# Optimization experiments

Measured on AMD Instinct MI355X. Metric: run time of the kernel, lower is better.

The kernel has to match this reference:

```python
import jax, jax.numpy as jnp
import numpy as np
import math

IN_DIM = 128
OUT_DIM = 128
EDGE_DIM = 16
LN_EPS = 1e-5


def setup_inputs() -> dict:
    key = jax.random.key(0)
    ks = jax.random.split(key, 6)
    bs, N = 8, 512
    x = jax.random.normal(ks[0], (bs, N, IN_DIM), dtype=jnp.float32)
    edge_feats = jax.random.normal(ks[1], (bs, N, N, EDGE_DIM), dtype=jnp.float32)
    # fc weight (out_dim, in_dim), xavier-uniform scale
    lim_w = math.sqrt(6.0 / (IN_DIM + OUT_DIM))
    W = jax.random.uniform(ks[2], (OUT_DIM, IN_DIM), minval=-lim_w, maxval=lim_w, dtype=jnp.float32)
    # attn_fc weight (1, 2*out_dim+edge_dim) split into a_src | a_dst | a_e
    fan_in = 2 * OUT_DIM + EDGE_DIM
    lim_a = math.sqrt(6.0 / (fan_in + 1))
    a = jax.random.uniform(ks[3], (fan_in,), minval=-lim_a, maxval=lim_a, dtype=jnp.float32)
    a_src, a_dst, a_e = a[:OUT_DIM], a[OUT_DIM:2 * OUT_DIM], a[2 * OUT_DIM:]
    gamma = jnp.ones((OUT_DIM,), dtype=jnp.float32)
    beta = jnp.zeros((OUT_DIM,), dtype=jnp.float32)
    return {"x": x, "edge_feats": edge_feats, "W": W, "a_src": a_src,
            "a_dst": a_dst, "a_e": a_e, "gamma": gamma, "beta": beta}


def reference(x, edge_feats, W, a_src, a_dst, a_e, gamma, beta):
    # h: (bs, N, out_dim)
    h = jnp.einsum('bni,oi->bno', x, W)
    scale = 1.0 / math.sqrt(OUT_DIM)
    # Decomposed rank-1 attention score: attn_fc([h_i, h_j, e_ij]) =
    # h_i.a_src + h_j.a_dst + e_ij.a_e  -- identical math, no (bs,N,N,2D+E) tensor.
    s_i = jnp.einsum('bnd,d->bn', h, a_src)           # row term (index i)
    s_j = jnp.einsum('bnd,d->bn', h, a_dst)           # col term (index j)
    s_e = jnp.einsum('bije,e->bij', edge_feats, a_e)  # edge term
    e_ij = (s_i[:, :, None] + s_j[:, None, :] + s_e) * scale  # (bs, N, N)
    # max-subtract then softmax over j (jax.nn.softmax is already max-stable,
    # and softmax(e - max) == softmax(e))
    alpha = jax.nn.softmax(e_ij, axis=-1)
    # weighted sum over neighbors j (dropout skipped: eval mode)
    h_prime = jnp.einsum('bij,bjd->bid', alpha, h)
    # LayerNorm over last dim
    mu = jnp.mean(h_prime, axis=-1, keepdims=True)
    var = jnp.var(h_prime, axis=-1, keepdims=True)
    out = (h_prime - mu) * jax.lax.rsqrt(var + LN_EPS) * gamma + beta
    return out
```

## Files before the change

### kernel.cpp

```cpp
#include <hip/hip_runtime.h>
#include <math.h>

#define NB 8
#define NN 512
#define D 128
#define TIF 4
#define K1R 8
#define LN_EPS 1e-5f
#define SCALE 0.08838834764831845f

typedef float f32x4 __attribute__((ext_vector_type(4)));

__device__ __forceinline__ float dotv(f32x4 a, f32x4 b) {
    f32x4 m = a * b;
    return m.x + m.y + m.z + m.w;
}
__device__ __forceinline__ float dot4(float4 a, float4 b) {
    return a.x * b.x + a.y * b.y + a.z * b.z + a.w * b.w;
}

__global__ __launch_bounds__(256) void k1_proj(
    const float* __restrict__ x, const float* __restrict__ W,
    const float* __restrict__ a_src, const float* __restrict__ a_dst,
    float* __restrict__ h_ws, float* __restrict__ si_ws, float* __restrict__ sj_ws)
{
    __shared__ __align__(16) float4 Wl[128][32];
    __shared__ __align__(16) float4 xl[K1R][32];
    __shared__ float redk[K1R][2][2];

    const int t = threadIdx.x;
    const int row0 = blockIdx.x * K1R;

    const float4* Wg = (const float4*)W;
#pragma unroll
    for (int k = 0; k < 16; ++k) {
        const int f = t + 256 * k;
        const int o = f >> 5, q = f & 31;
        Wl[o][q ^ (o & 7)] = Wg[f];
    }
    xl[t >> 5][t & 31] = ((const float4*)(x + (size_t)row0 * D))[t];
    __syncthreads();

    const int o = t & 127;
    const int rb = (t >> 7) * (K1R / 2);
    float acc[K1R / 2] = {0.f, 0.f, 0.f, 0.f};
#pragma unroll
    for (int q = 0; q < 32; ++q) {
        const float4 wv = Wl[o][q ^ (o & 7)];
#pragma unroll
        for (int r = 0; r < K1R / 2; ++r) acc[r] += dot4(wv, xl[rb + r][q]);
    }
    const float as = a_src[o], ad = a_dst[o];
#pragma unroll
    for (int r = 0; r < K1R / 2; ++r) {
        h_ws[(size_t)(row0 + rb + r) * D + o] = acc[r];
        float vs = acc[r] * as, vd = acc[r] * ad;
#pragma unroll
        for (int m = 32; m >= 1; m >>= 1) {
            vs += __shfl_xor(vs, m);
            vd += __shfl_xor(vd, m);
        }
        if ((t & 63) == 0) {
            redk[rb + r][0][(t >> 6) & 1] = vs;
            redk[rb + r][1][(t >> 6) & 1] = vd;
        }
    }
    __syncthreads();
    if (t < K1R) si_ws[row0 + t] = redk[t][0][0] + redk[t][0][1];
    else if (t < 2 * K1R) {
        const int r = t - K1R;
        sj_ws[row0 + r] = redk[r][1][0] + redk[r][1][1];
    }
}

__global__ __launch_bounds__(256, 4) void kfused(
    const float* __restrict__ ef, const float* __restrict__ a_e,
    const float* __restrict__ gamma, const float* __restrict__ beta,
    const float* __restrict__ h_ws, const float* __restrict__ si_ws,
    const float* __restrict__ sj_ws, float* __restrict__ out)
{
    __shared__ float sj_l[NN];
    __shared__ __align__(16) float sa[TIF][NN];
    __shared__ __align__(16) float part[4][TIF][D];
    __shared__ float redm[TIF][2];
    __shared__ float reds[TIF][2];

    const int t = threadIdx.x;
    const int w = t >> 6;
    const int lane = t & 63;
    const int bid = blockIdx.x;
    const int b = bid >> 7;
    const int i0 = (bid & 127) * TIF;

    sj_l[t] = sj_ws[b * NN + t];
    sj_l[t + 256] = sj_ws[b * NN + t + 256];

    const int c = t & 3;
    const f32x4 A = ((const f32x4*)a_e)[c];
    const f32x4* ef4 = (const f32x4*)ef + ((size_t)b * NN + i0) * NN * 4;
    float* saf = &sa[0][0];
#pragma unroll 8
    for (int k = 0; k < 32; ++k) {
        const int f = 256 * k + t;
        const f32x4 v = ef4[f];
        float p = dotv(v, A);
        p += __shfl_xor(p, 1);
        p += __shfl_xor(p, 2);
        if (c == 0) saf[f >> 2] = p;
    }
    __syncthreads();

    const int q = t & 127;
    const int rp = t >> 7;
    const int r0 = 2 * rp, r1 = 2 * rp + 1;
    const int wh = (t >> 6) & 1;
    const float si0 = si_ws[b * NN + i0 + r0];
    const float si1 = si_ws[b * NN + i0 + r1];
    const f32x4 sjv = *(const f32x4*)&sj_l[4 * q];
    const f32x4 e0 = (si0 + sjv + *(const f32x4*)&sa[r0][4 * q]) * SCALE;
    const f32x4 e1 = (si1 + sjv + *(const f32x4*)&sa[r1][4 * q]) * SCALE;
    float m0 = fmaxf(fmaxf(e0.x, e0.y), fmaxf(e0.z, e0.w));
    float m1 = fmaxf(fmaxf(e1.x, e1.y), fmaxf(e1.z, e1.w));
#pragma unroll
    for (int mm = 32; mm >= 1; mm >>= 1) {
        m0 = fmaxf(m0, __shfl_xor(m0, mm));
        m1 = fmaxf(m1, __shfl_xor(m1, mm));
    }
    if (lane == 0) { redm[r0][wh] = m0; redm[r1][wh] = m1; }
    __syncthreads();

    {
        const float mx0 = fmaxf(redm[r0][0], redm[r0][1]);
        const float mx1 = fmaxf(redm[r1][0], redm[r1][1]);
        f32x4 a0, a1;
        a0.x = __expf(e0.x - mx0); a0.y = __expf(e0.y - mx0);
        a0.z = __expf(e0.z - mx0); a0.w = __expf(e0.w - mx0);
        a1.x = __expf(e1.x - mx1); a1.y = __expf(e1.y - mx1);
        a1.z = __expf(e1.z - mx1); a1.w = __expf(e1.w - mx1);
        *(f32x4*)&sa[r0][4 * q] = a0;
        *(f32x4*)&sa[r1][4 * q] = a1;
        float s0 = a0.x + a0.y + a0.z + a0.w;
        float s1 = a1.x + a1.y + a1.z + a1.w;
#pragma unroll
        for (int mm = 32; mm >= 1; mm >>= 1) {
            s0 += __shfl_xor(s0, mm);
            s1 += __shfl_xor(s1, mm);
        }
        if (lane == 0) { reds[r0][wh] = s0; reds[r1][wh] = s1; }
    }
    __syncthreads();

    const int dl = (t & 31) << 2;
    const int g = t >> 5;
    float acc[TIF][4];
#pragma unroll
    for (int r = 0; r < TIF; ++r)
#pragma unroll
        for (int cc = 0; cc < 4; ++cc) acc[r][cc] = 0.f;

    const float* hb = h_ws + (size_t)b * NN * D;
#pragma unroll 2
    for (int jt = 0; jt < 16; ++jt) {
        const int j0 = (g << 6) + (jt << 2);
        float4 hv0 = *(const float4*)(hb + (size_t)(j0 + 0) * D + dl);
        float4 hv1 = *(const float4*)(hb + (size_t)(j0 + 1) * D + dl);
        float4 hv2 = *(const float4*)(hb + (size_t)(j0 + 2) * D + dl);
        float4 hv3 = *(const float4*)(hb + (size_t)(j0 + 3) * D + dl);
#pragma unroll
        for (int r = 0; r < TIF; ++r) {
            const f32x4 av = *(const f32x4*)&sa[r][j0];
            acc[r][0] += av.x * hv0.x + av.y * hv1.x + av.z * hv2.x + av.w * hv3.x;
            acc[r][1] += av.x * hv0.y + av.y * hv1.y + av.z * hv2.y + av.w * hv3.y;
            acc[r][2] += av.x * hv0.z + av.y * hv1.z + av.z * hv2.z + av.w * hv3.z;
            acc[r][3] += av.x * hv0.w + av.y * hv1.w + av.z * hv2.w + av.w * hv3.w;
        }
    }
#pragma unroll
    for (int r = 0; r < TIF; ++r)
#pragma unroll
        for (int cc = 0; cc < 4; ++cc) acc[r][cc] += __shfl_xor(acc[r][cc], 32);
    if (lane < 32) {
#pragma unroll
        for (int r = 0; r < TIF; ++r)
            *(float4*)&part[w][r][dl] = make_float4(acc[r][0], acc[r][1], acc[r][2], acc[r][3]);
    }
    __syncthreads();

    {
        const int r = w;
        const float inv = 1.0f / (reds[r][0] + reds[r][1]);
        const int d0 = lane, d1 = lane + 64;
        float v0 = 0.f, v1 = 0.f;
#pragma unroll
        for (int pw = 0; pw < 4; ++pw) {
            v0 += part[pw][r][d0];
            v1 += part[pw][r][d1];
        }
        v0 *= inv; v1 *= inv;
        float s = v0 + v1, qq = v0 * v0 + v1 * v1;
#pragma unroll
        for (int mm = 32; mm >= 1; mm >>= 1) {
            s += __shfl_xor(s, mm);
            qq += __shfl_xor(qq, mm);
        }
        const float mu = s * (1.f / 128.f);
        const float var = qq * (1.f / 128.f) - mu * mu;
        const float rs = rsqrtf(var + LN_EPS);
        const size_t ob = ((size_t)(b * NN + i0 + r)) * D;
        out[ob + d0] = (v0 - mu) * rs * gamma[d0] + beta[d0];
        out[ob + d1] = (v1 - mu) * rs * gamma[d1] + beta[d1];
    }
}

extern "C" void kernel_launch(void* const* d_in, const int* in_sizes, int n_in,
                              void* d_out, int out_size, void* d_ws, size_t ws_size,
                              hipStream_t stream) {
    const float* x     = (const float*)d_in[0];
    const float* ef    = (const float*)d_in[1];
    const float* W     = (const float*)d_in[2];
    const float* a_src = (const float*)d_in[3];
    const float* a_dst = (const float*)d_in[4];
    const float* a_e   = (const float*)d_in[5];
    const float* gamma = (const float*)d_in[6];
    const float* beta  = (const float*)d_in[7];
    float* out = (float*)d_out;

    float* h_ws  = (float*)d_ws;
    float* si_ws = h_ws + (size_t)NB * NN * D;
    float* sj_ws = si_ws + NB * NN;

    k1_proj<<<NB * NN / K1R, 256, 0, stream>>>(x, W, a_src, a_dst, h_ws, si_ws, sj_ws);
    kfused<<<NB * NN / TIF, 256, 0, stream>>>(ef, a_e, gamma, beta,
                                              h_ws, si_ws, sj_ws, out);
}
```

Baseline: 55.43 us.

## Stream edge features in chunks with online softmax and register prefetch

The fused attention kernel now walks the 512 neighbors in 64-wide chunks. It applies an online (flash-style) softmax with running max and sum, and rescales the accumulators per chunk. Edge-feature loads for the next chunk are prefetched into registers while the current chunk's scores, exponentials and h-weighted sums are computed, so the big edge tensor read overlaps with compute instead of completing before it. The trade is two barriers per chunk (16 total) plus extra rescale multiplies, in exchange for less shared memory and overlap of the dominant memory stream.

```diff
diff --git a/kernel.cpp b/kernel.cpp
--- a/kernel.cpp
+++ b/kernel.cpp
@@ -5,6 +5,8 @@
 #define NN 512
 #define D 128
 #define TIF 4
+#define JC 64
+#define NCK (NN / JC)
 #define K1R 8
 #define LN_EPS 1e-5f
 #define SCALE 0.08838834764831845f
@@ -80,10 +82,10 @@
     const float* __restrict__ sj_ws, float* __restrict__ out)
 {
     __shared__ float sj_l[NN];
-    __shared__ __align__(16) float sa[TIF][NN];
+    __shared__ __align__(16) float sa[TIF][JC];
+    __shared__ __align__(16) float ab[TIF][JC];
+    __shared__ float fsc_l[TIF];
     __shared__ __align__(16) float part[4][TIF][D];
-    __shared__ float redm[TIF][2];
-    __shared__ float reds[TIF][2];
 
     const int t = threadIdx.x;
     const int w = t >> 6;
@@ -95,106 +97,123 @@
     sj_l[t] = sj_ws[b * NN + t];
     sj_l[t + 256] = sj_ws[b * NN + t + 256];
 
+    const float si0 = si_ws[b * NN + i0 + 0];
+    const float si1 = si_ws[b * NN + i0 + 1];
+    const float si2 = si_ws[b * NN + i0 + 2];
+    const float si3 = si_ws[b * NN + i0 + 3];
+    const float si_w = (t < 64) ? si0 : (t < 128) ? si1 : (t < 192) ? si2 : si3;
+
     const int c = t & 3;
     const f32x4 A = ((const f32x4*)a_e)[c];
     const f32x4* ef4 = (const f32x4*)ef + ((size_t)b * NN + i0) * NN * 4;
-    float* saf = &sa[0][0];
-#pragma unroll 8
-    for (int k = 0; k < 32; ++k) {
-        const int f = 256 * k + t;
-        const f32x4 v = ef4[f];
-        float p = dotv(v, A);
-        p += __shfl_xor(p, 1);
-        p += __shfl_xor(p, 2);
-        if (c == 0) saf[f >> 2] = p;
-    }
-    __syncthreads();
-
-    const int q = t & 127;
-    const int rp = t >> 7;
-    const int r0 = 2 * rp, r1 = 2 * rp + 1;
-    const int wh = (t >> 6) & 1;
-    const float si0 = si_ws[b * NN + i0 + r0];
-    const float si1 = si_ws[b * NN + i0 + r1];
-    const f32x4 sjv = *(const f32x4*)&sj_l[4 * q];
-    const f32x4 e0 = (si0 + sjv + *(const f32x4*)&sa[r0][4 * q]) * SCALE;
-    const f32x4 e1 = (si1 + sjv + *(const f32x4*)&sa[r1][4 * q]) * SCALE;
-    float m0 = fmaxf(fmaxf(e0.x, e0.y), fmaxf(e0.z, e0.w));
-    float m1 = fmaxf(fmaxf(e1.x, e1.y), fmaxf(e1.z, e1.w));
-#pragma unroll
-    for (int mm = 32; mm >= 1; mm >>= 1) {
-        m0 = fmaxf(m0, __shfl_xor(m0, mm));
-        m1 = fmaxf(m1, __shfl_xor(m1, mm));
-    }
-    if (lane == 0) { redm[r0][wh] = m0; redm[r1][wh] = m1; }
-    __syncthreads();
-
-    {
-        const float mx0 = fmaxf(redm[r0][0], redm[r0][1]);
-        const float mx1 = fmaxf(redm[r1][0], redm[r1][1]);
-        f32x4 a0, a1;
-        a0.x = __expf(e0.x - mx0); a0.y = __expf(e0.y - mx0);
-        a0.z = __expf(e0.z - mx0); a0.w = __expf(e0.w - mx0);
-        a1.x = __expf(e1.x - mx1); a1.y = __expf(e1.y - mx1);
-        a1.z = __expf(e1.z - mx1); a1.w = __expf(e1.w - mx1);
-        *(f32x4*)&sa[r0][4 * q] = a0;
-        *(f32x4*)&sa[r1][4 * q] = a1;
-        float s0 = a0.x + a0.y + a0.z + a0.w;
-        float s1 = a1.x + a1.y + a1.z + a1.w;
-#pragma unroll
-        for (int mm = 32; mm >= 1; mm >>= 1) {
-            s0 += __shfl_xor(s0, mm);
-            s1 += __shfl_xor(s1, mm);
-        }
-        if (lane == 0) { reds[r0][wh] = s0; reds[r1][wh] = s1; }
-    }
-    __syncthreads();
-
+
+    const int jj = t & 63;
     const int dl = (t & 31) << 2;
     const int g = t >> 5;
-    float acc[TIF][4];
-#pragma unroll
-    for (int r = 0; r < TIF; ++r)
-#pragma unroll
-        for (int cc = 0; cc < 4; ++cc) acc[r][cc] = 0.f;
-
     const float* hb = h_ws + (size_t)b * NN * D;
-#pragma unroll 2
-    for (int jt = 0; jt < 16; ++jt) {
-        const int j0 = (g << 6) + (jt << 2);
-        float4 hv0 = *(const float4*)(hb + (size_t)(j0 + 0) * D + dl);
-        float4 hv1 = *(const float4*)(hb + (size_t)(j0 + 1) * D + dl);
-        float4 hv2 = *(const float4*)(hb + (size_t)(j0 + 2) * D + dl);
-        float4 hv3 = *(const float4*)(hb + (size_t)(j0 + 3) * D + dl);
-#pragma unroll
-        for (int r = 0; r < TIF; ++r) {
-            const f32x4 av = *(const f32x4*)&sa[r][j0];
-            acc[r][0] += av.x * hv0.x + av.y * hv1.x + av.z * hv2.x + av.w * hv3.x;
-            acc[r][1] += av.x * hv0.y + av.y * hv1.y + av.z * hv2.y + av.w * hv3.y;
-            acc[r][2] += av.x * hv0.z + av.y * hv1.z + av.z * hv2.z + av.w * hv3.z;
-            acc[r][3] += av.x * hv0.w + av.y * hv1.w + av.z * hv2.w + av.w * hv3.w;
-        }
-    }
-#pragma unroll
-    for (int r = 0; r < TIF; ++r)
-#pragma unroll
-        for (int cc = 0; cc < 4; ++cc) acc[r][cc] += __shfl_xor(acc[r][cc], 32);
+
+    float m_reg = -1e30f, l_reg = 0.f;
+    f32x4 acc0 = {0.f, 0.f, 0.f, 0.f};
+    f32x4 acc1 = {0.f, 0.f, 0.f, 0.f};
+    f32x4 acc2 = {0.f, 0.f, 0.f, 0.f};
+    f32x4 acc3 = {0.f, 0.f, 0.f, 0.f};
+
+    f32x4 p0 = ef4[0 * 2048 + t];
+    f32x4 p1 = ef4[1 * 2048 + t];
+    f32x4 p2 = ef4[2 * 2048 + t];
+    f32x4 p3 = ef4[3 * 2048 + t];
+
+    for (int ck = 0; ck < NCK; ++ck) {
+        {
+            float d0 = dotv(p0, A), d1 = dotv(p1, A);
+            float d2 = dotv(p2, A), d3 = dotv(p3, A);
+            d0 += __shfl_xor(d0, 1); d0 += __shfl_xor(d0, 2);
+            d1 += __shfl_xor(d1, 1); d1 += __shfl_xor(d1, 2);
+            d2 += __shfl_xor(d2, 1); d2 += __shfl_xor(d2, 2);
+            d3 += __shfl_xor(d3, 1); d3 += __shfl_xor(d3, 2);
+            if (c == 0) {
+                const int jl = t >> 2;
+                sa[0][jl] = d0; sa[1][jl] = d1; sa[2][jl] = d2; sa[3][jl] = d3;
+            }
+        }
+        if (ck < NCK - 1) {
+            const int off = (ck + 1) * 256 + t;
+            p0 = ef4[0 * 2048 + off];
+            p1 = ef4[1 * 2048 + off];
+            p2 = ef4[2 * 2048 + off];
+            p3 = ef4[3 * 2048 + off];
+        }
+        asm volatile("s_waitcnt lgkmcnt(0)" ::: "memory");
+        __builtin_amdgcn_s_barrier();
+        __builtin_amdgcn_sched_barrier(0);
+
+        {
+            const float e = (si_w + sj_l[ck * JC + jj] + sa[w][jj]) * SCALE;
+            float mc = e;
+#pragma unroll
+            for (int mm = 32; mm >= 1; mm >>= 1) mc = fmaxf(mc, __shfl_xor(mc, mm));
+            const float mn = fmaxf(m_reg, mc);
+            const float fs = __expf(m_reg - mn);
+            m_reg = mn;
+            const float av = __expf(e - mn);
+            ab[w][jj] = av;
+            float ls = av;
+#pragma unroll
+            for (int mm = 32; mm >= 1; mm >>= 1) ls += __shfl_xor(ls, mm);
+            l_reg = l_reg * fs + ls;
+            if (lane == 0) fsc_l[w] = fs;
+        }
+        asm volatile("s_waitcnt lgkmcnt(0)" ::: "memory");
+        __builtin_amdgcn_s_barrier();
+        __builtin_amdgcn_sched_barrier(0);
+
+        {
+            const float f0 = fsc_l[0], f1 = fsc_l[1];
+            const float f2 = fsc_l[2], f3 = fsc_l[3];
+            acc0 *= f0; acc1 *= f1; acc2 *= f2; acc3 *= f3;
+#pragma unroll
+            for (int jt = 0; jt < 2; ++jt) {
+                const int jl = (g << 3) + (jt << 2);
+                const int jg = ck * JC + jl;
+                const f32x4 hv0 = *(const f32x4*)(hb + (size_t)(jg + 0) * D + dl);
+                const f32x4 hv1 = *(const f32x4*)(hb + (size_t)(jg + 1) * D + dl);
+                const f32x4 hv2 = *(const f32x4*)(hb + (size_t)(jg + 2) * D + dl);
+                const f32x4 hv3 = *(const f32x4*)(hb + (size_t)(jg + 3) * D + dl);
+                const f32x4 a0v = *(const f32x4*)&ab[0][jl];
+                const f32x4 a1v = *(const f32x4*)&ab[1][jl];
+                const f32x4 a2v = *(const f32x4*)&ab[2][jl];
+                const f32x4 a3v = *(const f32x4*)&ab[3][jl];
+                acc0 += hv0 * a0v.x + hv1 * a0v.y + hv2 * a0v.z + hv3 * a0v.w;
+                acc1 += hv0 * a1v.x + hv1 * a1v.y + hv2 * a1v.z + hv3 * a1v.w;
+                acc2 += hv0 * a2v.x + hv1 * a2v.y + hv2 * a2v.z + hv3 * a2v.w;
+                acc3 += hv0 * a3v.x + hv1 * a3v.y + hv2 * a3v.z + hv3 * a3v.w;
+            }
+        }
+    }
+
+#pragma unroll
+    for (int cc = 0; cc < 4; ++cc) {
+        acc0[cc] += __shfl_xor(acc0[cc], 32);
+        acc1[cc] += __shfl_xor(acc1[cc], 32);
+        acc2[cc] += __shfl_xor(acc2[cc], 32);
+        acc3[cc] += __shfl_xor(acc3[cc], 32);
+    }
     if (lane < 32) {
-#pragma unroll
-        for (int r = 0; r < TIF; ++r)
-            *(float4*)&part[w][r][dl] = make_float4(acc[r][0], acc[r][1], acc[r][2], acc[r][3]);
+        *(f32x4*)&part[w][0][dl] = acc0;
+        *(f32x4*)&part[w][1][dl] = acc1;
+        *(f32x4*)&part[w][2][dl] = acc2;
+        *(f32x4*)&part[w][3][dl] = acc3;
     }
     __syncthreads();
 
     {
-        const int r = w;
-        const float inv = 1.0f / (reds[r][0] + reds[r][1]);
+        const float inv = 1.0f / l_reg;
         const int d0 = lane, d1 = lane + 64;
         float v0 = 0.f, v1 = 0.f;
 #pragma unroll
         for (int pw = 0; pw < 4; ++pw) {
-            v0 += part[pw][r][d0];
-            v1 += part[pw][r][d1];
+            v0 += part[pw][w][d0];
+            v1 += part[pw][w][d1];
         }
         v0 *= inv; v1 *= inv;
         float s = v0 + v1, qq = v0 * v0 + v1 * v1;
@@ -206,7 +225,7 @@
         const float mu = s * (1.f / 128.f);
         const float var = qq * (1.f / 128.f) - mu * mu;
         const float rs = rsqrtf(var + LN_EPS);
-        const size_t ob = ((size_t)(b * NN + i0 + r)) * D;
+        const size_t ob = ((size_t)(b * NN + i0 + w)) * D;
         out[ob + d0] = (v0 - mu) * rs * gamma[d0] + beta[d0];
         out[ob + d1] = (v1 - mu) * rs * gamma[d1] + beta[d1];
     }
```

Measured after the change: 51.45 us. 7.2% less time.
